# Optimization experiments

Hardware: AMD Instinct MI355X
Metric: run time of the kernel (lower is better)

Reference implementation:

```python
import jax, jax.numpy as jnp
import numpy as np

B, SEQ, PRED, ENC = 32, 720, 96, 321
LAYERS, SCALE = 2, 2
SEG = [48, 24]
D = [512, 256]
SNX = [SEQ // s for s in SEG]   # [15, 30]
SNY = [PRED // s for s in SEG]  # [2, 4]


def _gru(x, h, Wih, Whh, bih, bhh):
    # torch.nn.GRUCell math
    gi = x @ Wih.T + bih
    gh = h @ Whh.T + bhh
    i_r, i_z, i_n = jnp.split(gi, 3, axis=-1)
    h_r, h_z, h_n = jnp.split(gh, 3, axis=-1)
    r = jax.nn.sigmoid(i_r + h_r)
    z = jax.nn.sigmoid(i_z + h_z)
    n = jnp.tanh(i_n + r * h_n)
    return (1.0 - z) * n + z * h


def setup_inputs():
    key = jax.random.key(0)
    ks = iter(jax.random.split(key, 40))
    inp = {"x": jax.random.normal(next(ks), (B, SEQ, ENC), jnp.float32)}
    sc = 0.02
    for i in range(LAYERS):
        d, s = D[i], SEG[i]
        inp[f"W_emb{i}"] = jax.random.normal(next(ks), (d, s), jnp.float32) * sc
        inp[f"b_emb{i}"] = jnp.zeros((d,), jnp.float32)
        inp[f"Wih{i}"] = jax.random.normal(next(ks), (3 * d, d), jnp.float32) * sc
        inp[f"Whh{i}"] = jax.random.normal(next(ks), (3 * d, d), jnp.float32) * sc
        inp[f"bih{i}"] = jnp.zeros((3 * d,), jnp.float32)
        inp[f"bhh{i}"] = jnp.zeros((3 * d,), jnp.float32)
        inp[f"Wpred{i}"] = jax.random.normal(next(ks), (s, d), jnp.float32) * sc
        inp[f"bpred{i}"] = jnp.zeros((s,), jnp.float32)
        inp[f"pos{i}"] = jax.random.normal(next(ks), (SNY[i], d // 2), jnp.float32)
        inp[f"chan{i}"] = jax.random.normal(next(ks), (ENC, d // 2), jnp.float32)
    return inp


def _forward(x, params):
    seq_last = jax.lax.stop_gradient(x[:, -1:, :])   # [B,1,ENC] (detached in torch)
    xc = (x - seq_last).transpose(0, 2, 1)            # [B,ENC,SEQ]
    out = jnp.zeros((B, PRED, ENC), x.dtype)
    for i in range(LAYERS):
        p = params[i]
        d, s, T, S = D[i], SEG[i], SNX[i], SNY[i]
        # value embedding: [B*ENC, T, seg_len] -> [B*ENC, T, d]
        xe = jax.nn.relu(jnp.einsum('nts,ds->ntd', xc.reshape(-1, T, s), p['W_emb']) + p['b_emb'])
        if i == 0:
            seq = xe.transpose(1, 0, 2)   # all seg_num_x[0] segments in order
        else:
            # faithful to source: finer layer always consumes segments 0..scale^(i+1)-1
            # once per outer step, seg_num_x[0] times in total
            k = SCALE ** (i + 1)
            idx = np.tile(np.arange(k), SNX[0])
            seq = xe[:, idx].transpose(1, 0, 2)
        h0 = jnp.zeros((xe.shape[0], d), x.dtype)
        step = lambda h, xt: (_gru(xt, h, p['Wih'], p['Whh'], p['bih'], p['bhh']), None)
        h_fin, _ = jax.lax.scan(step, h0, seq)   # [B*ENC, d]
        # decoder: seg_num_y independent GRU cell applications (no carried state)
        half = d // 2
        pos = jnp.concatenate([
            jnp.broadcast_to(p['pos'][None], (ENC, S, half)),
            jnp.broadcast_to(p['chan'][:, None], (ENC, S, half))], axis=-1).reshape(ENC * S, d)
        pos = jnp.tile(pos, (B, 1)).reshape(S, B * ENC, d)   # contiguous chunks per step
        hn = jnp.repeat(h_fin, S, axis=0).reshape(S, B * ENC, d)
        hy = _gru(pos, hn, p['Wih'], p['Whh'], p['bih'], p['bhh'])   # [S, B*ENC, d]
        y = hy.reshape(S * B * ENC, d) @ p['Wpred'].T + p['bpred']   # [S*B*ENC, seg_len]
        y = y.reshape(-1, ENC, PRED).transpose(0, 2, 1)              # [B, PRED, ENC]
        out = out + y + seq_last
    return out / LAYERS


def reference(x, W_emb0, b_emb0, Wih0, Whh0, bih0, bhh0, Wpred0, bpred0, pos0, chan0,
              W_emb1, b_emb1, Wih1, Whh1, bih1, bhh1, Wpred1, bpred1, pos1, chan1):
    params = [
        dict(W_emb=W_emb0, b_emb=b_emb0, Wih=Wih0, Whh=Whh0, bih=bih0, bhh=bhh0,
             Wpred=Wpred0, bpred=bpred0, pos=pos0, chan=chan0),
        dict(W_emb=W_emb1, b_emb=b_emb1, Wih=Wih1, Whh=Whh1, bih=bih1, bhh=bhh1,
             Wpred=Wpred1, bpred=bpred1, pos=pos1, chan=chan1),
    ]
    return _forward(x, params)
```

## Files before the change

### kernel.cpp

```cpp
#include <hip/hip_runtime.h>
#include <math.h>


#define NB     10272
#define MP     10368
#define ENC_   321
#define SEQ_   720
#define PRED_  96
#define BATCH_ 32

typedef long long i64;
typedef unsigned short u16;
typedef unsigned int u32;
using bf16x8 = __attribute__((ext_vector_type(8))) short;
using f32x4  = __attribute__((ext_vector_type(4))) float;
using u16x4  = __attribute__((ext_vector_type(4))) unsigned short;

#define AS1 __attribute__((address_space(1)))
#define AS3 __attribute__((address_space(3)))
#define GLOAD16(g, l) __builtin_amdgcn_global_load_lds((const AS1 void*)(g), (AS3 void*)(l), 16, 0, 0)
#define MFMA16(a, b, c) __builtin_amdgcn_mfma_f32_16x16x32_bf16(a, b, c, 0, 0, 0)

__device__ __forceinline__ float bf2f(u16 u) {
    union { u32 i; float f; } v; v.i = ((u32)u) << 16; return v.f;
}
__device__ __forceinline__ u16 f2bf(float f) {
    union { float f; u32 i; } v; v.f = f;
    return (u16)((v.i + 0x7fff + ((v.i >> 16) & 1)) >> 16);
}
__device__ __forceinline__ float sigf(float x) {
    x = fminf(fmaxf(x, -30.f), 30.f);
    return 1.f / (1.f + __expf(-x));
}
__device__ __forceinline__ float tanhfast(float x) {
    x = fminf(fmaxf(x, -15.f), 15.f);
    float e = __expf(2.f * x);
    return (e - 1.f) / (e + 1.f);
}
__device__ __forceinline__ void swz(int idx, int NXT, int NYT, int& mt, int& nt) {
    int per = NYT * 8;
    int grp = idx / per;
    int base = grp * 8;
    int mg = NXT - base; if (mg > 8) mg = 8;
    int rem = idx - grp * per;
    mt = base + rem % mg;
    nt = rem / mg;
}

__global__ __launch_bounds__(256) void zero_bf(u16* __restrict__ b, i64 n) {
    i64 i = (i64)blockIdx.x * 256 + threadIdx.x;
    i64 n2 = n >> 1;
    if (i < n2) ((u32*)b)[i] = 0;
}

__global__ __launch_bounds__(256) void convert_pad(const float* __restrict__ src,
                                                   u16* __restrict__ dst,
                                                   int R, int C, int Rp, int Cp) {
    i64 idx = (i64)blockIdx.x * 256 + threadIdx.x;
    i64 total = (i64)Rp * Cp;
    if (idx >= total) return;
    int r = (int)(idx / Cp);
    int c = (int)(idx - (i64)r * Cp);
    dst[idx] = (r < R && c < C) ? f2bf(src[(i64)r * C + c]) : (u16)0;
}

__global__ __launch_bounds__(256) void seg_gather_bf(const float* __restrict__ x,
                                                     u16* __restrict__ dst,
                                                     int t0, int T, int s, int Kp) {
    i64 idx = (i64)blockIdx.x * 256 + threadIdx.x;
    i64 per_t = (i64)MP * Kp;
    i64 total = (i64)T * per_t;
    if (idx >= total) return;
    int t = (int)(idx / per_t);
    i64 rem = idx - (i64)t * per_t;
    int j = (int)(rem / MP);
    int n = (int)(rem - (i64)j * MP);
    float v = 0.f;
    if (n < NB && j < s) {
        int b = n / ENC_, e = n - b * ENC_;
        const float* xb = x + (i64)b * SEQ_ * ENC_ + e;
        v = xb[(i64)((t0 + t) * s + j) * ENC_] - xb[(i64)(SEQ_ - 1) * ENC_];
    }
    dst[((i64)t * MP + n) * Kp + j] = f2bf(v);
}

__global__ __launch_bounds__(256) void pmat_fill_bf(const float* __restrict__ pos,
                                                    const float* __restrict__ chan,
                                                    u16* __restrict__ dst,
                                                    int S, int d, int Rp) {
    i64 idx = (i64)blockIdx.x * 256 + threadIdx.x;
    i64 total = (i64)Rp * d;
    if (idx >= total) return;
    int row = (int)(idx / d);
    int c = (int)(idx - (i64)row * d);
    float v = 0.f;
    if (row < ENC_ * S) {
        int e = row / S, sy = row - e * S;
        int half = d >> 1;
        v = (c < half) ? pos[sy * half + c] : chan[e * half + (c - half)];
    }
    dst[idx] = f2bf(v);
}

__global__ __launch_bounds__(256) void out_kernel(const float* __restrict__ x,
                                                  const float* __restrict__ y0,
                                                  const float* __restrict__ y1,
                                                  float* __restrict__ out) {
    int idx = blockIdx.x * 256 + threadIdx.x;
    const int total = BATCH_ * PRED_ * ENC_;
    if (idx >= total) return;
    int b = idx / (PRED_ * ENC_);
    int r = idx - b * (PRED_ * ENC_);
    int p = r / ENC_;
    int e = r - p * ENC_;
    int n = b * ENC_ + e;
    float sl = x[(i64)b * SEQ_ * ENC_ + (i64)(SEQ_ - 1) * ENC_ + e];
    out[idx] = sl + 0.5f * (y0[(i64)n * PRED_ + p] + y1[(i64)n * PRED_ + p]);
}

template<int MODE>
__global__ __launch_bounds__(256) void gemm_bf16mfma(const u16* __restrict__ A,
                                                     const u16* __restrict__ B,
                                                     const float* __restrict__ bias,
                                                     void* __restrict__ Cp,
                                                     int K, int Mstore, int Nstore,
                                                     int ldc, int NXT, int NYT) {
    __shared__ u16 smA[128 * 64];
    __shared__ u16 smB[128 * 64];
    const int tid = threadIdx.x;
    const int w = tid >> 6, l = tid & 63;
    int mt, nt; swz(blockIdx.x, NXT, NYT, mt, nt);
    const int m0 = mt * 128, n0 = nt * 128;
    const int srow = (l >> 3) & 7, pch = l & 7;
    const int cch = pch ^ srow;
    const u16* ga[4]; const u16* gb[4];
#pragma unroll
    for (int r = 0; r < 4; ++r) {
        int seg = r * 4 + w;
        ga[r] = A + (i64)(m0 + seg * 8 + srow) * K + cch * 8;
        gb[r] = B + (i64)(n0 + seg * 8 + srow) * K + cch * 8;
    }
    f32x4 acc[4][4] = {};
    const int lr = l & 15, lg = l >> 4;
    const int wm = (w >> 1) * 64, wn = (w & 1) * 64;
    for (int kk = 0; kk < K; kk += 64) {
#pragma unroll
        for (int r = 0; r < 4; ++r) { GLOAD16(ga[r], smA + (r * 4 + w) * 512); ga[r] += 64; }
#pragma unroll
        for (int r = 0; r < 4; ++r) { GLOAD16(gb[r], smB + (r * 4 + w) * 512); gb[r] += 64; }
        __syncthreads();
#pragma unroll
        for (int s = 0; s < 2; ++s) {
            const int ph = ((s * 4 + lg) ^ (lr & 7)) * 8;
            bf16x8 av[4], bv[4];
#pragma unroll
            for (int i = 0; i < 4; ++i)
                av[i] = *(const bf16x8*)(smA + (wm + i * 16 + lr) * 64 + ph);
#pragma unroll
            for (int j = 0; j < 4; ++j)
                bv[j] = *(const bf16x8*)(smB + (wn + j * 16 + lr) * 64 + ph);
#pragma unroll
            for (int i = 0; i < 4; ++i)
#pragma unroll
                for (int j = 0; j < 4; ++j)
                    acc[i][j] = MFMA16(av[i], bv[j], acc[i][j]);
        }
        __syncthreads();
    }
    if (MODE == 3) {
        const int NCTG = ldc >> 4;
#pragma unroll
        for (int i = 0; i < 4; ++i) {
            int mt16 = (m0 + wm + i * 16) >> 4;
#pragma unroll
            for (int j = 0; j < 4; ++j) {
                int cb = n0 + wn + j * 16;
                if (cb >= Nstore) continue;
                float bs = bias[cb + lr];
                u16x4 sv;
#pragma unroll
                for (int r = 0; r < 4; ++r) sv[r] = f2bf(acc[i][j][r] + bs);
                *(u16x4*)((u16*)Cp + ((i64)mt16 * NCTG + (cb >> 4)) * 256 + l * 4) = sv;
            }
        }
        return;
    }
#pragma unroll
    for (int i = 0; i < 4; ++i) {
        int mbase = m0 + wm + i * 16 + 4 * lg;
#pragma unroll
        for (int j = 0; j < 4; ++j) {
            int c = n0 + wn + j * 16 + lr;
            if (c >= Nstore) continue;
            float bs = bias[c];
#pragma unroll
            for (int r = 0; r < 4; ++r) {
                int mm = mbase + r;
                if (mm < Mstore) {
                    float v = acc[i][j][r] + bs;
                    if (MODE == 2) v = fmaxf(v, 0.f);
                    if (MODE == 0) ((float*)Cp)[(i64)mm * ldc + c] = v;
                    else           ((u16*)Cp)[(i64)mm * ldc + c] = f2bf(v);
                }
            }
        }
    }
}

template<int D>
__device__ __forceinline__ void gru_step_body(const u16* __restrict__ xe,
                                              const u16* __restrict__ hsrc,
                                              const u16* __restrict__ Wih,
                                              const u16* __restrict__ Whh,
                                              const float* __restrict__ bih,
                                              const float* __restrict__ bhh,
                                              u16* __restrict__ hdst,
                                              int bx, int by,
                                              u16* smA, u16* smB, u16* smH) {
    const int tid = threadIdx.x;
    const int w = tid >> 6, l = tid & 63;
    const int m0 = bx * 64;
    const int c0 = by * 64;
    const int srow = (l >> 3) & 7, pch = l & 7;
    const int cch = pch ^ srow;
    const int lr = l & 15, lg = l >> 4;
    f32x4 aR[4] = {}, aZ[4] = {}, aNI[4] = {}, aNH[4] = {};
#pragma unroll
    for (int phase = 0; phase < 2; ++phase) {
        const u16* Abase = phase ? hsrc : xe;
        const u16* Bbase = phase ? Whh : Wih;
        const u16* ga[2]; const u16* gb[6];
#pragma unroll
        for (int r = 0; r < 2; ++r)
            ga[r] = Abase + (i64)(m0 + (r * 4 + w) * 8 + srow) * D + cch * 8;
#pragma unroll
        for (int q = 0; q < 6; ++q) {
            int gs = q * 4 + w;
            int g = gs >> 3, sp = gs & 7;
            gb[q] = Bbase + (i64)(g * D + c0 + sp * 8 + srow) * D + cch * 8;
        }
        for (int kk = 0; kk < D; kk += 64) {
#pragma unroll
            for (int r = 0; r < 2; ++r) GLOAD16(ga[r], smA + (r * 4 + w) * 512);
            if (phase == 1 && kk == c0) {
#pragma unroll
                for (int r = 0; r < 2; ++r) GLOAD16(ga[r], smH + (r * 4 + w) * 512);
            }
#pragma unroll
            for (int r = 0; r < 2; ++r) ga[r] += 64;
#pragma unroll
            for (int q = 0; q < 6; ++q) { GLOAD16(gb[q], smB + (q * 4 + w) * 512); gb[q] += 64; }
            __syncthreads();
#pragma unroll
            for (int s = 0; s < 2; ++s) {
                const int phs = ((s * 4 + lg) ^ (lr & 7)) * 8;
                bf16x8 av = *(const bf16x8*)(smA + (w * 16 + lr) * 64 + phs);
#pragma unroll
                for (int j = 0; j < 4; ++j) {
                    bf16x8 b0 = *(const bf16x8*)(smB + 0 * 4096 + (j * 16 + lr) * 64 + phs);
                    bf16x8 b1 = *(const bf16x8*)(smB + 1 * 4096 + (j * 16 + lr) * 64 + phs);
                    bf16x8 b2 = *(const bf16x8*)(smB + 2 * 4096 + (j * 16 + lr) * 64 + phs);
                    aR[j] = MFMA16(av, b0, aR[j]);
                    aZ[j] = MFMA16(av, b1, aZ[j]);
                    if (phase == 0)
                        aNI[j] = MFMA16(av, b2, aNI[j]);
                    else
                        aNH[j] = MFMA16(av, b2, aNH[j]);
                }
            }
            __syncthreads();
        }
    }
    const int rowb = m0 + w * 16 + 4 * lg;
#pragma unroll
    for (int j = 0; j < 4; ++j) {
        const int cc = c0 + j * 16 + lr;
        float bR = bih[cc] + bhh[cc];
        float bZ = bih[D + cc] + bhh[D + cc];
        float bNI = bih[2 * D + cc];
        float bNH = bhh[2 * D + cc];
#pragma unroll
        for (int r = 0; r < 4; ++r) {
            const int lrow = w * 16 + 4 * lg + r;
            const int lcol = j * 16 + lr;
            float ho = bf2f(smH[lrow * 64 + ((((lcol >> 3)) ^ (lrow & 7)) << 3) + (lcol & 7)]);
            float rr = sigf(aR[j][r] + bR);
            float zz = sigf(aZ[j][r] + bZ);
            float nn = tanhfast(aNI[j][r] + bNI + rr * (aNH[j][r] + bNH));
            hdst[(i64)(rowb + r) * D + cc] = f2bf((1.f - zz) * nn + zz * ho);
        }
    }
}

template<int D>
__device__ __forceinline__ void gru_step_h_body(const u16* __restrict__ gi,
                                                const u16* __restrict__ hsrc,
                                                const u16* __restrict__ Whh,
                                                const float* __restrict__ bhh,
                                                u16* __restrict__ hdst,
                                                int bx, int by,
                                                u16* smA, u16* smB, u16* smH) {
    constexpr int NCT = D / 16;
    constexpr int NCTG = 3 * D / 16;
    const int tid = threadIdx.x;
    const int w = tid >> 6, l = tid & 63;
    const int m0 = bx * 64;
    const int c0 = by * 64;
    const int srow = (l >> 3) & 7, pch = l & 7;
    const int cch = pch ^ srow;
    const int lr = l & 15, lg = l >> 4;
    f32x4 aR[4] = {}, aZ[4] = {}, aNH[4] = {};
    const u16* ga[2]; const u16* gb[6];
#pragma unroll
    for (int r = 0; r < 2; ++r)
        ga[r] = hsrc + (i64)(m0 + (r * 4 + w) * 8 + srow) * D + cch * 8;
#pragma unroll
    for (int q = 0; q < 6; ++q) {
        int gs = q * 4 + w;
        int g = gs >> 3, sp = gs & 7;
        gb[q] = Whh + (i64)(g * D + c0 + sp * 8 + srow) * D + cch * 8;
    }
    const int Trow = (m0 >> 4) + w;
    const i64 gbase = (i64)Trow * NCTG * 256 + l * 4;
    u16x4 g0[4], g1[4], g2[4];
    for (int kk = 0; kk < D; kk += 64) {
#pragma unroll
        for (int r = 0; r < 2; ++r) GLOAD16(ga[r], smA + (r * 4 + w) * 512);
        if (kk == c0) {
#pragma unroll
            for (int r = 0; r < 2; ++r) GLOAD16(ga[r], smH + (r * 4 + w) * 512);
        }
#pragma unroll
        for (int r = 0; r < 2; ++r) ga[r] += 64;
#pragma unroll
        for (int q = 0; q < 6; ++q) { GLOAD16(gb[q], smB + (q * 4 + w) * 512); gb[q] += 64; }
        __syncthreads();
        if (kk == D - 64) {
#pragma unroll
            for (int j = 0; j < 4; ++j) {
                const int ct = (c0 >> 4) + j;
                g0[j] = *(const u16x4*)(gi + gbase + (i64)(0 * NCT + ct) * 256);
                g1[j] = *(const u16x4*)(gi + gbase + (i64)(1 * NCT + ct) * 256);
                g2[j] = *(const u16x4*)(gi + gbase + (i64)(2 * NCT + ct) * 256);
            }
        }
#pragma unroll
        for (int s = 0; s < 2; ++s) {
            const int phs = ((s * 4 + lg) ^ (lr & 7)) * 8;
            bf16x8 av = *(const bf16x8*)(smA + (w * 16 + lr) * 64 + phs);
#pragma unroll
            for (int j = 0; j < 4; ++j) {
                bf16x8 b0 = *(const bf16x8*)(smB + 0 * 4096 + (j * 16 + lr) * 64 + phs);
                bf16x8 b1 = *(const bf16x8*)(smB + 1 * 4096 + (j * 16 + lr) * 64 + phs);
                bf16x8 b2 = *(const bf16x8*)(smB + 2 * 4096 + (j * 16 + lr) * 64 + phs);
                aR[j] = MFMA16(av, b0, aR[j]);
                aZ[j] = MFMA16(av, b1, aZ[j]);
                aNH[j] = MFMA16(av, b2, aNH[j]);
            }
        }
        __syncthreads();
    }
    const int rowb = m0 + w * 16 + 4 * lg;
#pragma unroll
    for (int j = 0; j < 4; ++j) {
        const int cc = c0 + j * 16 + lr;
        float bR = bhh[cc];
        float bZ = bhh[D + cc];
        float bNH = bhh[2 * D + cc];
#pragma unroll
        for (int r = 0; r < 4; ++r) {
            const int lrow = w * 16 + 4 * lg + r;
            const int lcol = j * 16 + lr;
            float ho = bf2f(smH[lrow * 64 + ((((lcol >> 3)) ^ (lrow & 7)) << 3) + (lcol & 7)]);
            float rr = sigf(bf2f(g0[j][r]) + aR[j][r] + bR);
            float zz = sigf(bf2f(g1[j][r]) + aZ[j][r] + bZ);
            float nn = tanhfast(bf2f(g2[j][r]) + rr * (aNH[j][r] + bNH));
            hdst[(i64)(rowb + r) * D + cc] = f2bf((1.f - zz) * nn + zz * ho);
        }
    }
}

template<int D>
__global__ __launch_bounds__(256, 3) void gru_step_h(const u16* __restrict__ gi,
                                                     const u16* __restrict__ hsrc,
                                                     const u16* __restrict__ Whh,
                                                     const float* __restrict__ bhh,
                                                     u16* __restrict__ hdst) {
    __shared__ u16 smA[64 * 64];
    __shared__ u16 smB[3 * 64 * 64];
    __shared__ u16 smH[64 * 64];
    gru_step_h_body<D>(gi, hsrc, Whh, bhh, hdst, blockIdx.x, blockIdx.y, smA, smB, smH);
}

__global__ __launch_bounds__(256, 3) void gru_step_comb(
    const u16* __restrict__ xe0, const u16* __restrict__ h0src,
    const u16* __restrict__ Wih0, const u16* __restrict__ Whh0,
    const float* __restrict__ bih0, const float* __restrict__ bhh0,
    u16* __restrict__ h0dst,
    const u16* __restrict__ gi1, const u16* __restrict__ h1src,
    const u16* __restrict__ Whh1, const float* __restrict__ bhh1,
    u16* __restrict__ h1dst) {
    __shared__ u16 smA[64 * 64];
    __shared__ u16 smB[3 * 64 * 64];
    __shared__ u16 smH[64 * 64];
    if (blockIdx.y < 8)
        gru_step_body<512>(xe0, h0src, Wih0, Whh0, bih0, bhh0, h0dst,
                           blockIdx.x, blockIdx.y, smA, smB, smH);
    else
        gru_step_h_body<256>(gi1, h1src, Whh1, bhh1, h1dst,
                             blockIdx.x, blockIdx.y - 8, smA, smB, smH);
}

template<int D, int S>
__global__ __launch_bounds__(256) void gru_dec(const u16* __restrict__ Asrc,
                                               const u16* __restrict__ Whh,
                                               const float* __restrict__ bhh,
                                               const u16* __restrict__ gi,
                                               u16* __restrict__ hy) {
    constexpr int NYT = D / 64;
    __shared__ u16 smA[128 * 64];
    __shared__ u16 smB[3 * 64 * 64];
    const int tid = threadIdx.x;
    const int w = tid >> 6, l = tid & 63;
    int mt, nt; swz(blockIdx.x, 81, NYT, mt, nt);
    const int m0 = mt * 128;
    const int c0 = nt * 64;
    const int srow = (l >> 3) & 7, pch = l & 7;
    const int cch = pch ^ srow;
    const u16* ga[4]; const u16* gb[6];
#pragma unroll
    for (int r = 0; r < 4; ++r)
        ga[r] = Asrc + (i64)(m0 + (r * 4 + w) * 8 + srow) * D + cch * 8;
#pragma unroll
    for (int q = 0; q < 6; ++q) {
        int gs = q * 4 + w;
        int g = gs >> 3, sp = gs & 7;
        gb[q] = Whh + (i64)(g * D + c0 + sp * 8 + srow) * D + cch * 8;
    }
    f32x4 acc[3][4][2] = {};
    const int lr = l & 15, lg = l >> 4;
    const int wm = (w >> 1) * 64, wc = (w & 1) * 32;
    for (int kk = 0; kk < D; kk += 64) {
#pragma unroll
        for (int r = 0; r < 4; ++r) { GLOAD16(ga[r], smA + (r * 4 + w) * 512); ga[r] += 64; }
#pragma unroll
        for (int q = 0; q < 6; ++q) { GLOAD16(gb[q], smB + (q * 4 + w) * 512); gb[q] += 64; }
        __syncthreads();
#pragma unroll
        for (int s = 0; s < 2; ++s) {
            const int ph = ((s * 4 + lg) ^ (lr & 7)) * 8;
            bf16x8 av[4], bv[3][2];
#pragma unroll
            for (int i = 0; i < 4; ++i)
                av[i] = *(const bf16x8*)(smA + (wm + i * 16 + lr) * 64 + ph);
#pragma unroll
            for (int g = 0; g < 3; ++g)
#pragma unroll
                for (int j = 0; j < 2; ++j)
                    bv[g][j] = *(const bf16x8*)(smB + g * 4096 + (wc + j * 16 + lr) * 64 + ph);
#pragma unroll
            for (int g = 0; g < 3; ++g)
#pragma unroll
                for (int i = 0; i < 4; ++i)
#pragma unroll
                    for (int j = 0; j < 2; ++j)
                        acc[g][i][j] = MFMA16(av[i], bv[g][j], acc[g][i][j]);
        }
        __syncthreads();
    }
#pragma unroll
    for (int i = 0; i < 4; ++i) {
        const int rowb = m0 + wm + 16 * i + 4 * lg;
        int e0 = rowb % ENC_;
#pragma unroll
        for (int j = 0; j < 2; ++j) {
            const int cc = c0 + wc + 16 * j + lr;
            float b0 = bhh[cc], b1 = bhh[D + cc], b2 = bhh[2 * D + cc];
#pragma unroll
            for (int r = 0; r < 4; ++r) {
                int mm = rowb + r;
                if (mm >= NB) continue;
                int e = e0 + r; if (e >= ENC_) e -= ENC_;
                float ho = bf2f(Asrc[(i64)mm * D + cc]);
                float hr = acc[0][i][j][r] + b0;
                float hz = acc[1][i][j][r] + b1;
                float hn2 = acc[2][i][j][r] + b2;
#pragma unroll
                for (int sy = 0; sy < S; ++sy) {
                    i64 gib = (i64)(e * S + sy) * 3 * D + cc;
                    float rr = sigf(bf2f(gi[gib]) + hr);
                    float zz = sigf(bf2f(gi[gib + D]) + hz);
                    float nn = tanhfast(bf2f(gi[gib + 2 * D]) + rr * hn2);
                    hy[((i64)mm * S + sy) * D + cc] = f2bf((1.f - zz) * nn + zz * ho);
                }
            }
        }
    }
}

extern "C" void kernel_launch(void* const* d_in, const int* in_sizes, int n_in,
                              void* d_out, int out_size, void* d_ws, size_t ws_size,
                              hipStream_t stream) {
    const float* x      = (const float*)d_in[0];
    const float* W_emb0 = (const float*)d_in[1];
    const float* b_emb0 = (const float*)d_in[2];
    const float* Wih0   = (const float*)d_in[3];
    const float* Whh0   = (const float*)d_in[4];
    const float* bih0   = (const float*)d_in[5];
    const float* bhh0   = (const float*)d_in[6];
    const float* Wpred0 = (const float*)d_in[7];
    const float* bpred0 = (const float*)d_in[8];
    const float* pos0   = (const float*)d_in[9];
    const float* chan0  = (const float*)d_in[10];
    const float* W_emb1 = (const float*)d_in[11];
    const float* b_emb1 = (const float*)d_in[12];
    const float* Wih1   = (const float*)d_in[13];
    const float* Whh1   = (const float*)d_in[14];
    const float* bih1   = (const float*)d_in[15];
    const float* bhh1   = (const float*)d_in[16];
    const float* Wpred1 = (const float*)d_in[17];
    const float* bpred1 = (const float*)d_in[18];
    const float* pos1   = (const float*)d_in[19];
    const float* chan1  = (const float*)d_in[20];
    float* out = (float*)d_out;

    i64 off = 0;
    char* base = (char*)d_ws;
    auto alloc = [&](i64 bytes) -> void* {
        void* p = base + off; off += (bytes + 255) & ~(i64)255; return p;
    };
    u16*   f_mirA  = (u16*)  alloc((i64)MP * 512 * 2);
    u16*   f_mirB  = (u16*)  alloc((i64)MP * 512 * 2);
    u16*   f_m1A   = (u16*)  alloc((i64)MP * 256 * 2);
    u16*   f_m1B   = (u16*)  alloc((i64)MP * 256 * 2);
    u16*   wih0b   = (u16*)  alloc((i64)1536 * 512 * 2);
    u16*   whh0b   = (u16*)  alloc((i64)1536 * 512 * 2);
    u16*   wih1b   = (u16*)  alloc((i64)768 * 256 * 2);
    u16*   whh1b   = (u16*)  alloc((i64)768 * 256 * 2);
    u16*   we0b    = (u16*)  alloc((i64)512 * 64 * 2);
    u16*   we1b    = (u16*)  alloc((i64)256 * 64 * 2);
    u16*   wp0b    = (u16*)  alloc((i64)128 * 512 * 2);
    u16*   wp1b    = (u16*)  alloc((i64)128 * 256 * 2);
    u16*   f_pm0   = (u16*)  alloc((i64)768 * 512 * 2);
    u16*   f_pm1   = (u16*)  alloc((i64)1408 * 256 * 2);
    u16*   f_gidec = (u16*)  alloc((i64)768 * 1536 * 2);
    u16*   f_hy    = (u16*)  alloc((i64)4 * NB * 256 * 2);
    float* f_y0    = (float*)alloc((i64)NB * 96 * 4);
    float* f_y1    = (float*)alloc((i64)NB * 96 * 4);
    u16*   f_gi1   = (u16*)  alloc((i64)4 * MP * 768 * 2);
    i64 fixed = off;

    char* R = base + fixed;
    i64 a1 = (((i64)4 * MP * 64 * 2) + 255) & ~(i64)255;
    i64 a2 = (i64)4 * MP * 256 * 2;
    i64 R1 = a1 + a2;
    u16* f_seg1 = (u16*)R;
    u16* f_xe1  = (u16*)(R + a1);
    int gsz = 1;
    {
        const int cand[4] = {15, 5, 3, 2};
        for (int ii = 0; ii < 4; ++ii) {
            i64 need = (i64)cand[ii] * MP * (64 + 512) * 2 + 2 * 256;
            i64 tot = fixed + (need > R1 ? need : R1);
            if (tot <= (i64)ws_size) { gsz = cand[ii]; break; }
        }
    }
    u16* f_seg0 = (u16*)R;
    i64 s1 = (((i64)gsz * MP * 64 * 2) + 255) & ~(i64)255;
    u16* f_xe0 = (u16*)(R + s1);

    auto cvt = [&](const float* s, u16* dst, int Rr, int C, int Rp, int Cp) {
        i64 tot = (i64)Rp * Cp;
        convert_pad<<<(int)((tot + 255) / 256), 256, 0, stream>>>(s, dst, Rr, C, Rp, Cp);
    };
    auto gemmN = [&](const u16* A, const u16* B, const float* bias, void* C,
                     int gx, int Nc, int K, int Mstore, int ldc, int mode) {
        int NYT = (Nc + 127) / 128;
        dim3 g(gx * NYT);
        if (mode == 0)      gemm_bf16mfma<0><<<g, 256, 0, stream>>>(A, B, bias, C, K, Mstore, Nc, ldc, gx, NYT);
        else if (mode == 1) gemm_bf16mfma<1><<<g, 256, 0, stream>>>(A, B, bias, C, K, Mstore, Nc, ldc, gx, NYT);
        else if (mode == 2) gemm_bf16mfma<2><<<g, 256, 0, stream>>>(A, B, bias, C, K, Mstore, Nc, ldc, gx, NYT);
        else                gemm_bf16mfma<3><<<g, 256, 0, stream>>>(A, B, bias, C, K, Mstore, Nc, ldc, gx, NYT);
    };

    cvt(Wih0, wih0b, 1536, 512, 1536, 512);
    cvt(Whh0, whh0b, 1536, 512, 1536, 512);
    cvt(Wih1, wih1b, 768, 256, 768, 256);
    cvt(Whh1, whh1b, 768, 256, 768, 256);
    cvt(W_emb0, we0b, 512, 48, 512, 64);
    cvt(W_emb1, we1b, 256, 24, 256, 64);
    cvt(Wpred0, wp0b, 48, 512, 128, 512);
    cvt(Wpred1, wp1b, 24, 256, 128, 256);
    pmat_fill_bf<<<(int)(((i64)768 * 512 + 255) / 256), 256, 0, stream>>>(pos0, chan0, f_pm0, 2, 512, 768);
    pmat_fill_bf<<<(int)(((i64)1408 * 256 + 255) / 256), 256, 0, stream>>>(pos1, chan1, f_pm1, 4, 256, 1408);

    {
        i64 n0 = (i64)MP * 512;
        zero_bf<<<(int)((n0 / 2 + 255) / 256), 256, 0, stream>>>(f_mirA, n0);
        i64 n1 = (i64)MP * 256;
        zero_bf<<<(int)((n1 / 2 + 255) / 256), 256, 0, stream>>>(f_m1A, n1);
        i64 tot = (i64)4 * MP * 64;
        seg_gather_bf<<<(int)((tot + 255) / 256), 256, 0, stream>>>(x, f_seg1, 0, 4, 24, 64);
    }
    gemmN(f_seg1, we1b, b_emb1, f_xe1, 324, 256, 64, 4 * MP, 256, 2);
    gemmN(f_xe1, wih1b, bih1, f_gi1, 324, 768, 256, 4 * MP, 768, 3);

    for (int t0 = 0; t0 < 15;) {
        int g = 15 - t0 < gsz ? 15 - t0 : gsz;
        i64 tot = (i64)g * MP * 64;
        seg_gather_bf<<<(int)((tot + 255) / 256), 256, 0, stream>>>(x, f_seg0, t0, g, 48, 64);
        gemmN(f_seg0, we0b, b_emb0, f_xe0, g * 81, 512, 64, g * MP, 512, 2);
        for (int s = 0; s < g; ++s) {
            int tg = t0 + s;
            const u16* A0s = (tg & 1) ? f_mirB : f_mirA;
            u16* A0d = (tg & 1) ? f_mirA : f_mirB;
            const u16* A1s = (tg & 1) ? f_m1B : f_m1A;
            u16* A1d = (tg & 1) ? f_m1A : f_m1B;
            gru_step_comb<<<dim3(162, 12), 256, 0, stream>>>(
                f_xe0 + (i64)s * MP * 512, A0s, wih0b, whh0b, bih0, bhh0, A0d,
                f_gi1 + (i64)(tg & 3) * MP * 768, A1s, whh1b, bhh1, A1d);
        }
        t0 += g;
    }
    for (int t = 15; t < 60; ++t) {
        const u16* A1s = (t & 1) ? f_m1B : f_m1A;
        u16* A1d = (t & 1) ? f_m1A : f_m1B;
        gru_step_h<256><<<dim3(162, 4), 256, 0, stream>>>(
            f_gi1 + (i64)(t & 3) * MP * 768, A1s, whh1b, bhh1, A1d);
    }

    gemmN(f_pm0, wih0b, bih0, f_gidec, 6, 1536, 512, 642, 1536, 1);
    gru_dec<512, 2><<<dim3(81 * 8), 256, 0, stream>>>(
        f_mirB, whh0b, bhh0, f_gidec, f_hy);
    gemmN(f_hy, wp0b, bpred0, f_y0, 161, 48, 512, 2 * NB, 48, 0);

    gemmN(f_pm1, wih1b, bih1, f_gidec, 11, 768, 256, 1284, 768, 1);
    gru_dec<256, 4><<<dim3(81 * 4), 256, 0, stream>>>(
        f_m1A, whh1b, bhh1, f_gidec, f_hy);
    gemmN(f_hy, wp1b, bpred1, f_y1, 321, 24, 256, 4 * NB, 24, 0);

    out_kernel<<<(BATCH_ * PRED_ * ENC_ + 255) / 256, 256, 0, stream>>>(x, f_y0, f_y1, out);
}
```

Baseline: 2.016 ms.

## Overlap layer-0 decoder kernels with layer-1 recurrent steps via combined launches

Layer-0's decoder work (input-gate GEMM, GRU decode and prediction GEMM) is merged into the first three layer-1 recurrent step launches. Each launch splits its grid by block index between the two independent workloads. The aim is to fill idle GPU capacity during the small layer-1 step launches and drop three separate serial kernel launches. Shared memory becomes a pooled buffer sized for the larger body, and launch bounds lose the occupancy hint of 3, which may change register allocation for the step body.

```diff
diff --git a/kernel.cpp b/kernel.cpp
--- a/kernel.cpp
+++ b/kernel.cpp
@@ -119,17 +119,16 @@
 }
 
 template<int MODE>
-__global__ __launch_bounds__(256) void gemm_bf16mfma(const u16* __restrict__ A,
-                                                     const u16* __restrict__ B,
-                                                     const float* __restrict__ bias,
-                                                     void* __restrict__ Cp,
-                                                     int K, int Mstore, int Nstore,
-                                                     int ldc, int NXT, int NYT) {
-    __shared__ u16 smA[128 * 64];
-    __shared__ u16 smB[128 * 64];
+__device__ __forceinline__ void gemm_body(const u16* __restrict__ A,
+                                          const u16* __restrict__ B,
+                                          const float* __restrict__ bias,
+                                          void* __restrict__ Cp,
+                                          int K, int Mstore, int Nstore,
+                                          int ldc, int NXT, int NYT, int bid,
+                                          u16* smA, u16* smB) {
     const int tid = threadIdx.x;
     const int w = tid >> 6, l = tid & 63;
-    int mt, nt; swz(blockIdx.x, NXT, NYT, mt, nt);
+    int mt, nt; swz(bid, NXT, NYT, mt, nt);
     const int m0 = mt * 128, n0 = nt * 128;
     const int srow = (l >> 3) & 7, pch = l & 7;
     const int cch = pch ^ srow;
@@ -205,6 +204,18 @@
             }
         }
     }
+}
+
+template<int MODE>
+__global__ __launch_bounds__(256) void gemm_bf16mfma(const u16* __restrict__ A,
+                                                     const u16* __restrict__ B,
+                                                     const float* __restrict__ bias,
+                                                     void* __restrict__ Cp,
+                                                     int K, int Mstore, int Nstore,
+                                                     int ldc, int NXT, int NYT) {
+    __shared__ u16 smA[128 * 64];
+    __shared__ u16 smB[128 * 64];
+    gemm_body<MODE>(A, B, bias, Cp, K, Mstore, Nstore, ldc, NXT, NYT, blockIdx.x, smA, smB);
 }
 
 template<int D>
@@ -380,6 +391,92 @@
     }
 }
 
+template<int D, int S>
+__device__ __forceinline__ void gru_dec_body(const u16* __restrict__ Asrc,
+                                             const u16* __restrict__ Whh,
+                                             const float* __restrict__ bhh,
+                                             const u16* __restrict__ gi,
+                                             u16* __restrict__ hy, int bid,
+                                             u16* smA, u16* smB) {
+    constexpr int NYT = D / 64;
+    const int tid = threadIdx.x;
+    const int w = tid >> 6, l = tid & 63;
+    int mt, nt; swz(bid, 81, NYT, mt, nt);
+    const int m0 = mt * 128;
+    const int c0 = nt * 64;
+    const int srow = (l >> 3) & 7, pch = l & 7;
+    const int cch = pch ^ srow;
+    const u16* ga[4]; const u16* gb[6];
+#pragma unroll
+    for (int r = 0; r < 4; ++r)
+        ga[r] = Asrc + (i64)(m0 + (r * 4 + w) * 8 + srow) * D + cch * 8;
+#pragma unroll
+    for (int q = 0; q < 6; ++q) {
+        int gs = q * 4 + w;
+        int g = gs >> 3, sp = gs & 7;
+        gb[q] = Whh + (i64)(g * D + c0 + sp * 8 + srow) * D + cch * 8;
+    }
+    f32x4 acc[3][4][2] = {};
+    const int lr = l & 15, lg = l >> 4;
+    const int wm = (w >> 1) * 64, wc = (w & 1) * 32;
+    for (int kk = 0; kk < D; kk += 64) {
+#pragma unroll
+        for (int r = 0; r < 4; ++r) { GLOAD16(ga[r], smA + (r * 4 + w) * 512); ga[r] += 64; }
+#pragma unroll
+        for (int q = 0; q < 6; ++q) { GLOAD16(gb[q], smB + (q * 4 + w) * 512); gb[q] += 64; }
+        __syncthreads();
+#pragma unroll
+        for (int s = 0; s < 2; ++s) {
+            const int ph = ((s * 4 + lg) ^ (lr & 7)) * 8;
+            bf16x8 av[4], bv[3][2];
+#pragma unroll
+            for (int i = 0; i < 4; ++i)
+                av[i] = *(const bf16x8*)(smA + (wm + i * 16 + lr) * 64 + ph);
+#pragma unroll
+            for (int g = 0; g < 3; ++g)
+#pragma unroll
+                for (int j = 0; j < 2; ++j)
+                    bv[g][j] = *(const bf16x8*)(smB + g * 4096 + (wc + j * 16 + lr) * 64 + ph);
+#pragma unroll
+            for (int g = 0; g < 3; ++g)
+#pragma unroll
+                for (int i = 0; i < 4; ++i)
+#pragma unroll
+                    for (int j = 0; j < 2; ++j)
+                        acc[g][i][j] = MFMA16(av[i], bv[g][j], acc[g][i][j]);
+        }
+        __syncthreads();
+    }
+#pragma unroll
+    for (int i = 0; i < 4; ++i) {
+        const int rowb = m0 + wm + 16 * i + 4 * lg;
+        int e0 = rowb % ENC_;
+#pragma unroll
+        for (int j = 0; j < 2; ++j) {
+            const int cc = c0 + wc + 16 * j + lr;
+            float b0 = bhh[cc], b1 = bhh[D + cc], b2 = bhh[2 * D + cc];
+#pragma unroll
+            for (int r = 0; r < 4; ++r) {
+                int mm = rowb + r;
+                if (mm >= NB) continue;
+                int e = e0 + r; if (e >= ENC_) e -= ENC_;
+                float ho = bf2f(Asrc[(i64)mm * D + cc]);
+                float hr = acc[0][i][j][r] + b0;
+                float hz = acc[1][i][j][r] + b1;
+                float hn2 = acc[2][i][j][r] + b2;
+#pragma unroll
+                for (int sy = 0; sy < S; ++sy) {
+                    i64 gib = (i64)(e * S + sy) * 3 * D + cc;
+                    float rr = sigf(bf2f(gi[gib]) + hr);
+                    float zz = sigf(bf2f(gi[gib + D]) + hz);
+                    float nn = tanhfast(bf2f(gi[gib + 2 * D]) + rr * hn2);
+                    hy[((i64)mm * S + sy) * D + cc] = f2bf((1.f - zz) * nn + zz * ho);
+                }
+            }
+        }
+    }
+}
+
 template<int D>
 __global__ __launch_bounds__(256, 3) void gru_step_h(const u16* __restrict__ gi,
                                                      const u16* __restrict__ hsrc,
@@ -390,6 +487,17 @@
     __shared__ u16 smB[3 * 64 * 64];
     __shared__ u16 smH[64 * 64];
     gru_step_h_body<D>(gi, hsrc, Whh, bhh, hdst, blockIdx.x, blockIdx.y, smA, smB, smH);
+}
+
+template<int D, int S>
+__global__ __launch_bounds__(256) void gru_dec(const u16* __restrict__ Asrc,
+                                               const u16* __restrict__ Whh,
+                                               const float* __restrict__ bhh,
+                                               const u16* __restrict__ gi,
+                                               u16* __restrict__ hy) {
+    __shared__ u16 smA[128 * 64];
+    __shared__ u16 smB[3 * 64 * 64];
+    gru_dec_body<D, S>(Asrc, Whh, bhh, gi, hy, blockIdx.x, smA, smB);
 }
 
 __global__ __launch_bounds__(256, 3) void gru_step_comb(
@@ -411,90 +519,39 @@
                              blockIdx.x, blockIdx.y - 8, smA, smB, smH);
 }
 
-template<int D, int S>
-__global__ __launch_bounds__(256) void gru_dec(const u16* __restrict__ Asrc,
-                                               const u16* __restrict__ Whh,
-                                               const float* __restrict__ bhh,
-                                               const u16* __restrict__ gi,
-                                               u16* __restrict__ hy) {
-    constexpr int NYT = D / 64;
-    __shared__ u16 smA[128 * 64];
-    __shared__ u16 smB[3 * 64 * 64];
-    const int tid = threadIdx.x;
-    const int w = tid >> 6, l = tid & 63;
-    int mt, nt; swz(blockIdx.x, 81, NYT, mt, nt);
-    const int m0 = mt * 128;
-    const int c0 = nt * 64;
-    const int srow = (l >> 3) & 7, pch = l & 7;
-    const int cch = pch ^ srow;
-    const u16* ga[4]; const u16* gb[6];
-#pragma unroll
-    for (int r = 0; r < 4; ++r)
-        ga[r] = Asrc + (i64)(m0 + (r * 4 + w) * 8 + srow) * D + cch * 8;
-#pragma unroll
-    for (int q = 0; q < 6; ++q) {
-        int gs = q * 4 + w;
-        int g = gs >> 3, sp = gs & 7;
-        gb[q] = Whh + (i64)(g * D + c0 + sp * 8 + srow) * D + cch * 8;
-    }
-    f32x4 acc[3][4][2] = {};
-    const int lr = l & 15, lg = l >> 4;
-    const int wm = (w >> 1) * 64, wc = (w & 1) * 32;
-    for (int kk = 0; kk < D; kk += 64) {
-#pragma unroll
-        for (int r = 0; r < 4; ++r) { GLOAD16(ga[r], smA + (r * 4 + w) * 512); ga[r] += 64; }
-#pragma unroll
-        for (int q = 0; q < 6; ++q) { GLOAD16(gb[q], smB + (q * 4 + w) * 512); gb[q] += 64; }
-        __syncthreads();
-#pragma unroll
-        for (int s = 0; s < 2; ++s) {
-            const int ph = ((s * 4 + lg) ^ (lr & 7)) * 8;
-            bf16x8 av[4], bv[3][2];
-#pragma unroll
-            for (int i = 0; i < 4; ++i)
-                av[i] = *(const bf16x8*)(smA + (wm + i * 16 + lr) * 64 + ph);
-#pragma unroll
-            for (int g = 0; g < 3; ++g)
-#pragma unroll
-                for (int j = 0; j < 2; ++j)
-                    bv[g][j] = *(const bf16x8*)(smB + g * 4096 + (wc + j * 16 + lr) * 64 + ph);
-#pragma unroll
-            for (int g = 0; g < 3; ++g)
-#pragma unroll
-                for (int i = 0; i < 4; ++i)
-#pragma unroll
-                    for (int j = 0; j < 2; ++j)
-                        acc[g][i][j] = MFMA16(av[i], bv[g][j], acc[g][i][j]);
-        }
-        __syncthreads();
-    }
-#pragma unroll
-    for (int i = 0; i < 4; ++i) {
-        const int rowb = m0 + wm + 16 * i + 4 * lg;
-        int e0 = rowb % ENC_;
-#pragma unroll
-        for (int j = 0; j < 2; ++j) {
-            const int cc = c0 + wc + 16 * j + lr;
-            float b0 = bhh[cc], b1 = bhh[D + cc], b2 = bhh[2 * D + cc];
-#pragma unroll
-            for (int r = 0; r < 4; ++r) {
-                int mm = rowb + r;
-                if (mm >= NB) continue;
-                int e = e0 + r; if (e >= ENC_) e -= ENC_;
-                float ho = bf2f(Asrc[(i64)mm * D + cc]);
-                float hr = acc[0][i][j][r] + b0;
-                float hz = acc[1][i][j][r] + b1;
-                float hn2 = acc[2][i][j][r] + b2;
-#pragma unroll
-                for (int sy = 0; sy < S; ++sy) {
-                    i64 gib = (i64)(e * S + sy) * 3 * D + cc;
-                    float rr = sigf(bf2f(gi[gib]) + hr);
-                    float zz = sigf(bf2f(gi[gib + D]) + hz);
-                    float nn = tanhfast(bf2f(gi[gib + 2 * D]) + rr * hn2);
-                    hy[((i64)mm * S + sy) * D + cc] = f2bf((1.f - zz) * nn + zz * ho);
-                }
-            }
-        }
+template<int MODE>
+__global__ __launch_bounds__(256) void comb_gemm_step(
+    const u16* __restrict__ A, const u16* __restrict__ B,
+    const float* __restrict__ bias, void* __restrict__ Cp,
+    int K, int Mstore, int Nstore, int ldc, int NXT, int NYT, int G,
+    const u16* __restrict__ gi1, const u16* __restrict__ h1src,
+    const u16* __restrict__ Whh1, const float* __restrict__ bhh1,
+    u16* __restrict__ h1dst) {
+    __shared__ u16 pool[20480];
+    if ((int)blockIdx.x < G) {
+        gemm_body<MODE>(A, B, bias, Cp, K, Mstore, Nstore, ldc, NXT, NYT,
+                        blockIdx.x, pool, pool + 8192);
+    } else {
+        int idx = blockIdx.x - G;
+        gru_step_h_body<256>(gi1, h1src, Whh1, bhh1, h1dst, idx % 162, idx / 162,
+                             pool, pool + 4096, pool + 16384);
+    }
+}
+
+__global__ __launch_bounds__(256) void comb_dec_step(
+    const u16* __restrict__ Asrc, const u16* __restrict__ Whh0,
+    const float* __restrict__ bhh0, const u16* __restrict__ gidec,
+    u16* __restrict__ hy,
+    const u16* __restrict__ gi1, const u16* __restrict__ h1src,
+    const u16* __restrict__ Whh1, const float* __restrict__ bhh1,
+    u16* __restrict__ h1dst) {
+    __shared__ u16 pool[20480];
+    if (blockIdx.x < 648) {
+        gru_dec_body<512, 2>(Asrc, Whh0, bhh0, gidec, hy, blockIdx.x, pool, pool + 8192);
+    } else {
+        int idx = blockIdx.x - 648;
+        gru_step_h_body<256>(gi1, h1src, Whh1, bhh1, h1dst, idx % 162, idx / 162,
+                             pool, pool + 4096, pool + 16384);
     }
 }
 
@@ -622,18 +679,33 @@
         }
         t0 += g;
     }
-    for (int t = 15; t < 60; ++t) {
+
+    {
+        const u16* A1s = f_m1B; u16* A1d = f_m1A;
+        comb_gemm_step<1><<<dim3(72 + 648), 256, 0, stream>>>(
+            f_pm0, wih0b, bih0, f_gidec, 512, 642, 1536, 1536, 6, 12, 72,
+            f_gi1 + (i64)(15 & 3) * MP * 768, A1s, whh1b, bhh1, A1d);
+    }
+    {
+        const u16* A1s = f_m1A; u16* A1d = f_m1B;
+        comb_dec_step<<<dim3(648 + 648), 256, 0, stream>>>(
+            f_mirB, whh0b, bhh0, f_gidec, f_hy,
+            f_gi1 + (i64)(16 & 3) * MP * 768, A1s, whh1b, bhh1, A1d);
+    }
+    {
+        const u16* A1s = f_m1B; u16* A1d = f_m1A;
+        comb_gemm_step<0><<<dim3(161 + 648), 256, 0, stream>>>(
+            f_hy, wp0b, bpred0, f_y0, 512, 2 * NB, 48, 48, 161, 1, 161,
+            f_gi1 + (i64)(17 & 3) * MP * 768, A1s, whh1b, bhh1, A1d);
+    }
+
+    for (int t = 18; t < 60; ++t) {
         const u16* A1s = (t & 1) ? f_m1B : f_m1A;
         u16* A1d = (t & 1) ? f_m1A : f_m1B;
         gru_step_h<256><<<dim3(162, 4), 256, 0, stream>>>(
             f_gi1 + (i64)(t & 3) * MP * 768, A1s, whh1b, bhh1, A1d);
     }
 
-    gemmN(f_pm0, wih0b, bih0, f_gidec, 6, 1536, 512, 642, 1536, 1);
-    gru_dec<512, 2><<<dim3(81 * 8), 256, 0, stream>>>(
-        f_mirB, whh0b, bhh0, f_gidec, f_hy);
-    gemmN(f_hy, wp0b, bpred0, f_y0, 161, 48, 512, 2 * NB, 48, 0);
-
     gemmN(f_pm1, wih1b, bih1, f_gidec, 11, 768, 256, 1284, 768, 1);
     gru_dec<256, 4><<<dim3(81 * 4), 256, 0, stream>>>(
         f_m1A, whh1b, bhh1, f_gidec, f_hy);
```

Result: slower. 2.064 ms (+2.4%).
